# Kernel optimization log

Measured on AMD Instinct MI355X. Metric: run time of the kernel, lower is better.

Reference implementation:

```python
import jax, jax.numpy as jnp
import numpy as np

D_MODEL = 2048
N_HEADS = 16
HEAD_DIM = D_MODEL // N_HEADS
D_FF = ((int(8 * D_MODEL / 3) + 64) // 64) * 64  # 5504
B, T = 2, 2048
EPS = 1e-8
NEG = -1e9


def rotate_half(x):
    half = x.shape[-1] // 2
    return jnp.concatenate([-x[..., half:], x[..., :half]], axis=-1)


def apply_rope(x, cos, sin):
    # x: [B,H,T,hd]; cos/sin: [T,hd] -> [1,1,T,hd]
    c = cos[None, None, :, :]
    s = sin[None, None, :, :]
    return x * c + rotate_half(x) * s


def rmsnorm(x, w):
    rms = jnp.sqrt(jnp.mean(x * x, axis=-1, keepdims=True))
    return w * x / (rms + EPS)


def setup_inputs() -> dict:
    key = jax.random.key(0)
    ks = jax.random.split(key, 12)
    x = jax.random.normal(ks[0], (B, T, D_MODEL), dtype=jnp.float32)
    # RoPE tables
    inv_freq = 1.0 / (10000.0 ** (jnp.arange(0, HEAD_DIM, 2, dtype=jnp.float32) / HEAD_DIM))
    pos = jnp.arange(T, dtype=jnp.float32)
    freqs = pos[:, None] * inv_freq[None, :]          # [T, hd/2]
    emb = jnp.concatenate([freqs, freqs], axis=-1)    # [T, hd]
    cos, sin = jnp.cos(emb), jnp.sin(emb)
    # causal additive mask [T,T]
    mask = jnp.where(jnp.tril(jnp.ones((T, T), dtype=bool)), 0.0, NEG).astype(jnp.float32)
    scale = 0.02
    Wq = jax.random.normal(ks[1], (D_MODEL, D_MODEL), dtype=jnp.float32) * scale
    Wk = jax.random.normal(ks[2], (D_MODEL, D_MODEL), dtype=jnp.float32) * scale
    Wv = jax.random.normal(ks[3], (D_MODEL, D_MODEL), dtype=jnp.float32) * scale
    Wo = jax.random.normal(ks[4], (D_MODEL, D_MODEL), dtype=jnp.float32) * scale
    W1 = jax.random.normal(ks[5], (D_FF, D_MODEL), dtype=jnp.float32) * scale
    W2 = jax.random.normal(ks[6], (D_FF, D_MODEL), dtype=jnp.float32) * scale
    Wout = jax.random.normal(ks[7], (D_MODEL, D_FF), dtype=jnp.float32) * scale
    g1 = jnp.ones((D_MODEL,), dtype=jnp.float32)
    g2 = jnp.ones((D_MODEL,), dtype=jnp.float32)
    return {"x": x, "cos": cos, "sin": sin, "mask": mask,
            "g1": g1, "g2": g2, "Wq": Wq, "Wk": Wk, "Wv": Wv, "Wo": Wo,
            "W1": W1, "W2": W2, "Wout": Wout}


def reference(x, cos, sin, mask, g1, g2, Wq, Wk, Wv, Wo, W1, W2, Wout):
    Bb, Tt, Dd = x.shape

    def split_heads(t):  # [B,T,D] -> [B,H,T,hd]
        return t.reshape(Bb, Tt, N_HEADS, HEAD_DIM).transpose(0, 2, 1, 3)

    h = rmsnorm(x, g1)
    Q = apply_rope(split_heads(h @ Wq.T), cos, sin)
    K = apply_rope(split_heads(h @ Wk.T), cos, sin)
    V = split_heads(h @ Wv.T)
    scores = jnp.einsum('bhqd,bhkd->bhqk', Q, K) / jnp.sqrt(jnp.float32(HEAD_DIM))
    scores = scores + mask  # broadcast [T,T] over [B,H,T,T]
    weights = jax.nn.softmax(scores, axis=-1)
    attn = jnp.einsum('bhqk,bhkd->bhqd', weights, V)
    attn = attn.transpose(0, 2, 1, 3).reshape(Bb, Tt, Dd)
    x = x + attn @ Wo.T

    h2 = rmsnorm(x, g2)
    ff = (jax.nn.silu(h2 @ W1.T) * (h2 @ W2.T)) @ Wout.T
    return x + ff
```

## Files before the change

kernel.cpp:

```cpp
#include <hip/hip_runtime.h>


using bf16 = __bf16;
typedef __bf16 bf16x2 __attribute__((ext_vector_type(2)));
typedef __bf16 bf16x8 __attribute__((ext_vector_type(8)));
typedef float f32x4 __attribute__((ext_vector_type(4)));

#define MFMA_BF16(a, b, c) __builtin_amdgcn_mfma_f32_16x16x32_bf16((a), (b), (c), 0, 0, 0)

__device__ __forceinline__ void gld_lds16(const void* g, void* l) {
  __builtin_amdgcn_global_load_lds((const __attribute__((address_space(1))) void*)g,
                                   (__attribute__((address_space(3))) void*)l,
                                   16, 0, 0);
}

__global__ void detect_dtype(const unsigned int* __restrict__ X, int* __restrict__ flag) {
  const int tid = threadIdx.x;
  const unsigned int w = X[tid];
  const unsigned int e_lo = (w >> 7) & 0xFF;
  const unsigned int e_hi = (w >> 23) & 0xFF;
  const bool sane = (e_lo >= 97u && e_lo <= 157u) && (e_hi >= 97u && e_hi <= 157u);
  const unsigned long long m = __ballot(sane);
  if (tid == 0) *flag = (__popcll(m) > 48) ? 1 : 0;
}

__global__ __launch_bounds__(256) void convert_in(const void* __restrict__ src,
                                                  bf16* __restrict__ dst,
                                                  const int* __restrict__ flag) {
  const size_t i = ((size_t)blockIdx.x * 256 + threadIdx.x) * 8;
  if (*flag) {
    *(bf16x8*)(dst + i) = *(const bf16x8*)((const bf16*)src + i);
  } else {
    const float* s = (const float*)src;
    float4 a = *(const float4*)(s + i);
    float4 b = *(const float4*)(s + i + 4);
    bf16x8 o;
    o[0] = (bf16)a.x; o[1] = (bf16)a.y; o[2] = (bf16)a.z; o[3] = (bf16)a.w;
    o[4] = (bf16)b.x; o[5] = (bf16)b.y; o[6] = (bf16)b.z; o[7] = (bf16)b.w;
    *(bf16x8*)(dst + i) = o;
  }
}

__global__ __launch_bounds__(256) void rmsnorm_bf16(const bf16* __restrict__ X,
                                                    const bf16* __restrict__ g,
                                                    bf16* __restrict__ Hout) {
  const int row = blockIdx.x, tid = threadIdx.x;
  const size_t off = (size_t)row * 2048 + tid * 8;
  bf16x8 x8 = *(const bf16x8*)(X + off);
  float v[8];
  float s = 0.f;
#pragma unroll
  for (int j = 0; j < 8; ++j) { v[j] = (float)x8[j]; s += v[j] * v[j]; }
#pragma unroll
  for (int o = 32; o; o >>= 1) s += __shfl_xor(s, o);
  __shared__ float red[4];
  if ((tid & 63) == 0) red[tid >> 6] = s;
  __syncthreads();
  const float tot = red[0] + red[1] + red[2] + red[3];
  const float inv = 1.f / (sqrtf(tot * (1.f / 2048.f)) + 1e-8f);
  bf16x8 g8 = *(const bf16x8*)(g + tid * 8);
  bf16x8 o8;
#pragma unroll
  for (int j = 0; j < 8; ++j) o8[j] = (bf16)((float)g8[j] * v[j] * inv);
  *(bf16x8*)(Hout + off) = o8;
}

__global__ __launch_bounds__(256) void rmsnorm_f32(const float* __restrict__ X,
                                                   const bf16* __restrict__ g,
                                                   bf16* __restrict__ Hout) {
  const int row = blockIdx.x, tid = threadIdx.x;
  const size_t off = (size_t)row * 2048 + tid * 8;
  float4 a0 = *(const float4*)(X + off);
  float4 a1 = *(const float4*)(X + off + 4);
  float v[8] = {a0.x, a0.y, a0.z, a0.w, a1.x, a1.y, a1.z, a1.w};
  float s = 0.f;
#pragma unroll
  for (int j = 0; j < 8; ++j) s += v[j] * v[j];
#pragma unroll
  for (int o = 32; o; o >>= 1) s += __shfl_xor(s, o);
  __shared__ float red[4];
  if ((tid & 63) == 0) red[tid >> 6] = s;
  __syncthreads();
  const float tot = red[0] + red[1] + red[2] + red[3];
  const float inv = 1.f / (sqrtf(tot * (1.f / 2048.f)) + 1e-8f);
  bf16x8 g8 = *(const bf16x8*)(g + tid * 8);
  bf16x8 o8;
#pragma unroll
  for (int j = 0; j < 8; ++j) o8[j] = (bf16)((float)g8[j] * v[j] * inv);
  *(bf16x8*)(Hout + off) = o8;
}

__global__ __launch_bounds__(256) void rope_k(bf16* __restrict__ Q, bf16* __restrict__ Kg,
                                              const bf16* __restrict__ cosb,
                                              const bf16* __restrict__ sinb) {
  const int tid = threadIdx.x;
  const int rr = tid >> 7;
  const int c = tid & 127;
  const int bt = blockIdx.x * 2 + rr;
  const int t = bt & 2047;
  const int h = c >> 3;
  const int d0 = (c & 7) * 8;
  const size_t row = (size_t)bt * 2048;
  const int i0 = h * 128 + d0;
  bf16x8 c0 = *(const bf16x8*)(cosb + t * 128 + d0);
  bf16x8 c1 = *(const bf16x8*)(cosb + t * 128 + d0 + 64);
  bf16x8 s0 = *(const bf16x8*)(sinb + t * 128 + d0);
  bf16x8 s1 = *(const bf16x8*)(sinb + t * 128 + d0 + 64);
  bf16x8 qa = *(const bf16x8*)(Q + row + i0);
  bf16x8 qb = *(const bf16x8*)(Q + row + i0 + 64);
  bf16x8 ka = *(const bf16x8*)(Kg + row + i0);
  bf16x8 kb = *(const bf16x8*)(Kg + row + i0 + 64);
  bf16x8 qo0, qo1, ko0, ko1;
#pragma unroll
  for (int j = 0; j < 8; ++j) {
    float cj0 = (float)c0[j], cj1 = (float)c1[j];
    float sj0 = (float)s0[j], sj1 = (float)s1[j];
    float qaj = (float)qa[j], qbj = (float)qb[j];
    float kaj = (float)ka[j], kbj = (float)kb[j];
    qo0[j] = (bf16)(qaj * cj0 - qbj * sj0);
    qo1[j] = (bf16)(qbj * cj1 + qaj * sj1);
    ko0[j] = (bf16)(kaj * cj0 - kbj * sj0);
    ko1[j] = (bf16)(kbj * cj1 + kaj * sj1);
  }
  *(bf16x8*)(Q + row + i0) = qo0;
  *(bf16x8*)(Q + row + i0 + 64) = qo1;
  *(bf16x8*)(Kg + row + i0) = ko0;
  *(bf16x8*)(Kg + row + i0 + 64) = ko1;
}

template <int EPI>
__global__ __launch_bounds__(256) void gemm_bt(const bf16* __restrict__ A,
                                               const bf16* __restrict__ W,
                                               bf16* __restrict__ Cb, float* __restrict__ Cf,
                                               const bf16* __restrict__ resb,
                                               const float* __restrict__ resf,
                                               const bf16* __restrict__ mulb,
                                               const int* __restrict__ oflag,
                                               int M, int N, int K) {
  __shared__ bf16 As[2][128 * 32];
  __shared__ bf16 Ws[2][128 * 32];
  const int tid = threadIdx.x;
  const int wave = tid >> 6, lane = tid & 63;
  const int quad = lane >> 4, l15 = lane & 15;
  const int wm = wave >> 1, wn = wave & 1;
  const int m0 = blockIdx.y * 128, n0 = blockIdx.x * 128;

  f32x4 acc[4][4];
#pragma unroll
  for (int i = 0; i < 4; ++i)
#pragma unroll
    for (int j = 0; j < 4; ++j) acc[i][j] = {0.f, 0.f, 0.f, 0.f};

  const int srow = lane >> 2;
  const int skk = (lane & 3) * 8;
  const bf16* Ab = A + (size_t)m0 * K;
  const bf16* Wb = W + (size_t)n0 * K;

  auto stage = [&](int buf, int kb) {
    const int k0 = kb << 5;
#pragma unroll
    for (int c = 0; c < 2; ++c) {
      const int r = (wave * 2 + c) * 16 + srow;
      gld_lds16(Ab + (size_t)r * K + k0 + skk, (char*)As[buf] + (wave * 2 + c) * 1024);
      gld_lds16(Wb + (size_t)r * K + k0 + skk, (char*)Ws[buf] + (wave * 2 + c) * 1024);
    }
  };
  auto compute = [&](int buf) {
    bf16x8 af[4], wf[4];
#pragma unroll
    for (int mt = 0; mt < 4; ++mt)
      af[mt] = *(const bf16x8*)&As[buf][(wm * 64 + mt * 16 + l15) * 32 + quad * 8];
#pragma unroll
    for (int nt = 0; nt < 4; ++nt)
      wf[nt] = *(const bf16x8*)&Ws[buf][(wn * 64 + nt * 16 + l15) * 32 + quad * 8];
#pragma unroll
    for (int mt = 0; mt < 4; ++mt)
#pragma unroll
      for (int nt = 0; nt < 4; ++nt)
        acc[mt][nt] = MFMA_BF16(af[mt], wf[nt], acc[mt][nt]);
  };

  const int nk = K >> 5;
  stage(0, 0);
  for (int kb = 0; kb < nk; kb += 2) {
    __syncthreads();
    if (kb + 1 < nk) stage(1, kb + 1);
    compute(0);
    __syncthreads();
    if (kb + 2 < nk) stage(0, kb + 2);
    compute(1);
  }

  const int obf = (EPI == 4 && oflag) ? *oflag : 0;
#pragma unroll
  for (int mt = 0; mt < 4; ++mt) {
#pragma unroll
    for (int nt = 0; nt < 4; ++nt) {
#pragma unroll
      for (int r = 0; r < 4; ++r) {
        const int row = m0 + wm * 64 + mt * 16 + quad * 4 + r;
        const int col = n0 + wn * 64 + nt * 16 + l15;
        const size_t idx = (size_t)row * N + col;
        const float v = acc[mt][nt][r];
        if constexpr (EPI == 0) {
          Cb[idx] = (bf16)v;
        } else if constexpr (EPI == 1) {
          Cf[idx] = v + (float)resb[idx];
        } else if constexpr (EPI == 2) {
          Cb[idx] = (bf16)(v / (1.f + __expf(-v)));
        } else if constexpr (EPI == 3) {
          Cb[idx] = (bf16)((float)mulb[idx] * v);
        } else {
          const float rres = resf[idx] + v;
          if (obf) Cb[idx] = (bf16)rres;
          else     Cf[idx] = rres;
        }
      }
    }
  }
}

__global__ __launch_bounds__(256) void flash_attn(const bf16* __restrict__ Q,
                                                  const bf16* __restrict__ Kg,
                                                  const bf16* __restrict__ Vg,
                                                  bf16* __restrict__ O) {
  __shared__ bf16 Ks[2][64 * 128];
  __shared__ bf16 Vt[2][128 * 64];
  __shared__ bf16 Ps[4 * 16 * 64];
  const int tid = threadIdx.x;
  const int wave = tid >> 6, lane = tid & 63;
  const int quad = lane >> 4, l15 = lane & 15;
  const int bh = blockIdx.y;
  const int b = bh >> 4, h = bh & 15;
  const size_t base = (size_t)b * 2048 * 2048 + h * 128;
  const float scale = 0.08838834764831845f;

  bf16x8 vva[2], vvb[2];

  auto stageK = [&](int buf, int kb) {
    const int k0 = kb * 64;
#pragma unroll
    for (int c = 0; c < 4; ++c) {
      const int ch = tid + 256 * c;
      const int row = ch >> 4;
      const int scb = ((ch & 15) * 16) ^ ((row & 7) << 4);
      gld_lds16((const char*)(Kg + base + (size_t)(k0 + row) * 2048) + scb,
                (char*)Ks[buf] + wave * 1024 + c * 4096);
    }
  };
  auto loadV = [&](int kb) {
    const int k0 = kb * 64;
#pragma unroll
    for (int c = 0; c < 2; ++c) {
      const int tau = tid + 256 * c;
      const int kp = tau & 31;
      const int d0 = (tau >> 5) * 8;
      vva[c] = *(const bf16x8*)(Vg + base + (size_t)(k0 + 2 * kp) * 2048 + d0);
      vvb[c] = *(const bf16x8*)(Vg + base + (size_t)(k0 + 2 * kp + 1) * 2048 + d0);
    }
  };
  auto writeV = [&](int buf) {
#pragma unroll
    for (int c = 0; c < 2; ++c) {
      const int tau = tid + 256 * c;
      const int kp = tau & 31;
      const int d0 = (tau >> 5) * 8;
#pragma unroll
      for (int j = 0; j < 8; ++j) {
        bf16x2 pr = {vva[c][j], vvb[c][j]};
        const int d = d0 + j;
        *(bf16x2*)((char*)Vt[buf] + d * 128 + ((4 * kp) ^ ((d & 7) << 4))) = pr;
      }
    }
  };

#pragma unroll 1
  for (int half = 0; half < 2; ++half) {
    const int qt = half ? (31 - (int)blockIdx.x) : (int)blockIdx.x;
    const int q0 = qt * 64;

    bf16x8 qf[4];
    {
      const bf16* qrow = Q + base + (size_t)(q0 + wave * 16 + l15) * 2048;
#pragma unroll
      for (int ks = 0; ks < 4; ++ks) qf[ks] = *(const bf16x8*)(qrow + ks * 32 + quad * 8);
    }

    f32x4 o[8];
#pragma unroll
    for (int i = 0; i < 8; ++i) o[i] = {0.f, 0.f, 0.f, 0.f};
    float m_r[4] = {-1e30f, -1e30f, -1e30f, -1e30f};
    float l_r[4] = {0.f, 0.f, 0.f, 0.f};

    __syncthreads();
    loadV(0);
    stageK(0, 0);
    writeV(0);
    __syncthreads();
    if (qt >= 1) { loadV(1); stageK(1, 1); }

#pragma unroll 1
    for (int kb = 0; kb <= qt; ++kb) {
      const int cur = kb & 1;
      const int k0 = kb * 64;

      f32x4 s[4];
#pragma unroll
      for (int nt = 0; nt < 4; ++nt) {
        s[nt] = {0.f, 0.f, 0.f, 0.f};
        const int krow = nt * 16 + l15;
#pragma unroll
        for (int ks = 0; ks < 4; ++ks) {
          bf16x8 kf = *(const bf16x8*)((char*)Ks[cur] + krow * 256 +
                                       ((ks * 64 + quad * 16) ^ ((krow & 7) << 4)));
          s[nt] = MFMA_BF16(qf[ks], kf, s[nt]);
        }
      }

      float sv[4][4];
#pragma unroll
      for (int nt = 0; nt < 4; ++nt) {
#pragma unroll
        for (int r = 0; r < 4; ++r) {
          float v = s[nt][r] * scale;
          const int key = k0 + nt * 16 + l15;
          const int qq = q0 + wave * 16 + quad * 4 + r;
          if (key > qq) v = -1e9f;
          sv[nt][r] = v;
        }
      }

#pragma unroll
      for (int r = 0; r < 4; ++r) {
        float rmax = fmaxf(fmaxf(sv[0][r], sv[1][r]), fmaxf(sv[2][r], sv[3][r]));
#pragma unroll
        for (int off = 1; off < 16; off <<= 1) rmax = fmaxf(rmax, __shfl_xor(rmax, off));
        const float mnew = fmaxf(m_r[r], rmax);
        const float alpha = __expf(m_r[r] - mnew);
        float psum = 0.f;
        const int qrow = quad * 4 + r;
#pragma unroll
        for (int nt = 0; nt < 4; ++nt) {
          const float p = __expf(sv[nt][r] - mnew);
          psum += p;
          *(bf16*)((char*)Ps + wave * 2048 + qrow * 128 +
                   ((2 * (nt * 16 + l15)) ^ ((qrow & 7) << 4))) = (bf16)p;
        }
#pragma unroll
        for (int off = 1; off < 16; off <<= 1) psum += __shfl_xor(psum, off);
        l_r[r] = l_r[r] * alpha + psum;
        m_r[r] = mnew;
#pragma unroll
        for (int nt2 = 0; nt2 < 8; ++nt2) o[nt2][r] *= alpha;
      }

      asm volatile("s_waitcnt lgkmcnt(0)" ::: "memory");

#pragma unroll
      for (int ks2 = 0; ks2 < 2; ++ks2) {
        bf16x8 pf = *(const bf16x8*)((char*)Ps + wave * 2048 + l15 * 128 +
                                     ((ks2 * 64 + quad * 16) ^ ((l15 & 7) << 4)));
#pragma unroll
        for (int nt2 = 0; nt2 < 8; ++nt2) {
          const int drow = nt2 * 16 + l15;
          bf16x8 vf = *(const bf16x8*)((char*)Vt[cur] + drow * 128 +
                                       ((ks2 * 64 + quad * 16) ^ ((drow & 7) << 4)));
          o[nt2] = MFMA_BF16(pf, vf, o[nt2]);
        }
      }

      if (kb + 1 <= qt) writeV(cur ^ 1);

      __syncthreads();
      if (kb + 2 <= qt) { loadV(kb + 2); stageK(cur, kb + 2); }
    }

#pragma unroll
    for (int nt2 = 0; nt2 < 8; ++nt2) {
#pragma unroll
      for (int r = 0; r < 4; ++r) {
        const int qq = q0 + wave * 16 + quad * 4 + r;
        const int dd = nt2 * 16 + l15;
        O[base + (size_t)qq * 2048 + dd] = (bf16)(o[nt2][r] / l_r[r]);
      }
    }
  }
}

extern "C" void kernel_launch(void* const* d_in, const int* in_sizes, int n_in,
                              void* d_out, int out_size, void* d_ws, size_t ws_size,
                              hipStream_t stream) {
  const void* x_raw = d_in[0];
  const void* cos_raw = d_in[1];
  const void* sin_raw = d_in[2];
  const void* g1_raw = d_in[4];
  const void* g2_raw = d_in[5];
  const void* W_raw[7] = {d_in[6], d_in[7], d_in[8], d_in[9], d_in[10], d_in[11], d_in[12]};

  char* ws = (char*)d_ws;
  const size_t MB = 1048576ull;
  int* flag = (int*)ws;
  bf16* g1c = (bf16*)(ws + 4096);
  bf16* g2c = (bf16*)(ws + 12288);
  bf16* cosc = (bf16*)(ws + 65536);
  bf16* sinc = (bf16*)(ws + 655360);
  bf16* xc   = (bf16*)(ws + 2 * MB);
  bf16* wslot= (bf16*)(ws + 18 * MB);
  bf16* hbuf = (bf16*)(ws + 41 * MB);
  bf16* qbuf = (bf16*)(ws + 57 * MB);
  bf16* kbuf = (bf16*)(ws + 73 * MB);
  bf16* vbuf = (bf16*)(ws + 89 * MB);
  bf16* abuf = (bf16*)(ws + 105 * MB);
  float* x1  = (float*)(ws + 57 * MB);
  bf16* h2   = (bf16*)(ws + 41 * MB);
  bf16* ubuf = (bf16*)(ws + 89 * MB);

  const int M = 4096;
  dim3 blk(256);

  detect_dtype<<<1, 64, 0, stream>>>((const unsigned int*)x_raw, flag);

  convert_in<<<4096, blk, 0, stream>>>(x_raw, xc, flag);
  convert_in<<<128, blk, 0, stream>>>(cos_raw, cosc, flag);
  convert_in<<<128, blk, 0, stream>>>(sin_raw, sinc, flag);
  convert_in<<<1, blk, 0, stream>>>(g1_raw, g1c, flag);
  convert_in<<<1, blk, 0, stream>>>(g2_raw, g2c, flag);

  rmsnorm_bf16<<<M, blk, 0, stream>>>(xc, g1c, hbuf);

  convert_in<<<2048, blk, 0, stream>>>(W_raw[0], wslot, flag);
  gemm_bt<0><<<dim3(16, 32), blk, 0, stream>>>(hbuf, wslot, qbuf, nullptr, nullptr, nullptr, nullptr, nullptr, M, 2048, 2048);
  convert_in<<<2048, blk, 0, stream>>>(W_raw[1], wslot, flag);
  gemm_bt<0><<<dim3(16, 32), blk, 0, stream>>>(hbuf, wslot, kbuf, nullptr, nullptr, nullptr, nullptr, nullptr, M, 2048, 2048);
  convert_in<<<2048, blk, 0, stream>>>(W_raw[2], wslot, flag);
  gemm_bt<0><<<dim3(16, 32), blk, 0, stream>>>(hbuf, wslot, vbuf, nullptr, nullptr, nullptr, nullptr, nullptr, M, 2048, 2048);

  rope_k<<<M / 2, blk, 0, stream>>>(qbuf, kbuf, cosc, sinc);
  flash_attn<<<dim3(16, 32), blk, 0, stream>>>(qbuf, kbuf, vbuf, abuf);

  convert_in<<<2048, blk, 0, stream>>>(W_raw[3], wslot, flag);
  gemm_bt<1><<<dim3(16, 32), blk, 0, stream>>>(abuf, wslot, nullptr, x1, xc, nullptr, nullptr, nullptr, M, 2048, 2048);

  rmsnorm_f32<<<M, blk, 0, stream>>>(x1, g2c, h2);

  convert_in<<<5504, blk, 0, stream>>>(W_raw[4], wslot, flag);
  gemm_bt<2><<<dim3(43, 32), blk, 0, stream>>>(h2, wslot, ubuf, nullptr, nullptr, nullptr, nullptr, nullptr, M, 5504, 2048);
  convert_in<<<5504, blk, 0, stream>>>(W_raw[5], wslot, flag);
  gemm_bt<3><<<dim3(43, 32), blk, 0, stream>>>(h2, wslot, ubuf, nullptr, nullptr, nullptr, ubuf, nullptr, M, 5504, 2048);
  convert_in<<<5504, blk, 0, stream>>>(W_raw[6], wslot, flag);
  gemm_bt<4><<<dim3(16, 32), blk, 0, stream>>>(ubuf, wslot, (bf16*)d_out, (float*)d_out, nullptr, x1, nullptr, flag, M, 2048, 5504);
}
```

Before: 1.072 ms.

## Restructure flash attention pipeline with single V buffer and explicit waitcnt barriers

Reworks the flash attention K/V staging. V goes into a single LDS buffer that is written at the start of each iteration from registers prefetched one block ahead. K staging is issued after the mid-iteration barrier, and __syncthreads is replaced by raw s_barrier with explicit vmcnt/lgkmcnt waits, s_setprio around the MFMA sections, and sched_barriers. The launch grid is also swapped so blockIdx.x indexes batch-head and blockIdx.y the query tile, which changes dispatch order and L2 locality. This cuts LDS use and synchronization overhead, but the hand-counted vmcnt values are fragile and the single V buffer adds a barrier per iteration.

After: 991.4 us. -7.5%, faster.

```diff
diff --git a/kernel.cpp b/kernel.cpp
--- a/kernel.cpp
+++ b/kernel.cpp
@@ -225,12 +225,12 @@
                                                   const bf16* __restrict__ Vg,
                                                   bf16* __restrict__ O) {
   __shared__ bf16 Ks[2][64 * 128];
-  __shared__ bf16 Vt[2][128 * 64];
+  __shared__ bf16 Vt[128 * 64];
   __shared__ bf16 Ps[4 * 16 * 64];
   const int tid = threadIdx.x;
   const int wave = tid >> 6, lane = tid & 63;
   const int quad = lane >> 4, l15 = lane & 15;
-  const int bh = blockIdx.y;
+  const int bh = blockIdx.x;
   const int b = bh >> 4, h = bh & 15;
   const size_t base = (size_t)b * 2048 * 2048 + h * 128;
   const float scale = 0.08838834764831845f;
@@ -259,7 +259,7 @@
       vvb[c] = *(const bf16x8*)(Vg + base + (size_t)(k0 + 2 * kp + 1) * 2048 + d0);
     }
   };
-  auto writeV = [&](int buf) {
+  auto writeV = [&]() {
 #pragma unroll
     for (int c = 0; c < 2; ++c) {
       const int tau = tid + 256 * c;
@@ -269,14 +269,14 @@
       for (int j = 0; j < 8; ++j) {
         bf16x2 pr = {vva[c][j], vvb[c][j]};
         const int d = d0 + j;
-        *(bf16x2*)((char*)Vt[buf] + d * 128 + ((4 * kp) ^ ((d & 7) << 4))) = pr;
+        *(bf16x2*)((char*)Vt + d * 128 + ((4 * kp) ^ ((d & 7) << 4))) = pr;
       }
     }
   };
 
 #pragma unroll 1
   for (int half = 0; half < 2; ++half) {
-    const int qt = half ? (31 - (int)blockIdx.x) : (int)blockIdx.x;
+    const int qt = half ? (31 - (int)blockIdx.y) : (int)blockIdx.y;
     const int q0 = qt * 64;
 
     bf16x8 qf[4];
@@ -292,19 +292,23 @@
     float m_r[4] = {-1e30f, -1e30f, -1e30f, -1e30f};
     float l_r[4] = {0.f, 0.f, 0.f, 0.f};
 
-    __syncthreads();
     loadV(0);
     stageK(0, 0);
-    writeV(0);
-    __syncthreads();
-    if (qt >= 1) { loadV(1); stageK(1, 1); }
+    if (qt >= 1) stageK(1, 1);
+    asm volatile("s_waitcnt vmcnt(4)" ::: "memory");
+    __builtin_amdgcn_s_barrier();
+    __builtin_amdgcn_sched_barrier(0);
 
 #pragma unroll 1
     for (int kb = 0; kb <= qt; ++kb) {
       const int cur = kb & 1;
       const int k0 = kb * 64;
 
+      writeV();
+      if (kb + 1 <= qt) loadV(kb + 1);
+
       f32x4 s[4];
+      __builtin_amdgcn_s_setprio(1);
 #pragma unroll
       for (int nt = 0; nt < 4; ++nt) {
         s[nt] = {0.f, 0.f, 0.f, 0.f};
@@ -316,6 +320,7 @@
           s[nt] = MFMA_BF16(qf[ks], kf, s[nt]);
         }
       }
+      __builtin_amdgcn_s_setprio(0);
 
       float sv[4][4];
 #pragma unroll
@@ -355,7 +360,12 @@
       }
 
       asm volatile("s_waitcnt lgkmcnt(0)" ::: "memory");
-
+      __builtin_amdgcn_s_barrier();
+      __builtin_amdgcn_sched_barrier(0);
+
+      if (kb + 2 <= qt) stageK(cur, kb + 2);
+
+      __builtin_amdgcn_s_setprio(1);
 #pragma unroll
       for (int ks2 = 0; ks2 < 2; ++ks2) {
         bf16x8 pf = *(const bf16x8*)((char*)Ps + wave * 2048 + l15 * 128 +
@@ -363,16 +373,17 @@
 #pragma unroll
         for (int nt2 = 0; nt2 < 8; ++nt2) {
           const int drow = nt2 * 16 + l15;
-          bf16x8 vf = *(const bf16x8*)((char*)Vt[cur] + drow * 128 +
+          bf16x8 vf = *(const bf16x8*)((char*)Vt + drow * 128 +
                                        ((ks2 * 64 + quad * 16) ^ ((drow & 7) << 4)));
           o[nt2] = MFMA_BF16(pf, vf, o[nt2]);
         }
       }
-
-      if (kb + 1 <= qt) writeV(cur ^ 1);
-
-      __syncthreads();
-      if (kb + 2 <= qt) { loadV(kb + 2); stageK(cur, kb + 2); }
+      __builtin_amdgcn_s_setprio(0);
+
+      asm volatile("s_waitcnt lgkmcnt(0)" ::: "memory");
+      asm volatile("s_waitcnt vmcnt(8)" ::: "memory");
+      __builtin_amdgcn_s_barrier();
+      __builtin_amdgcn_sched_barrier(0);
     }
 
 #pragma unroll
@@ -436,7 +447,7 @@
   gemm_bt<0><<<dim3(16, 32), blk, 0, stream>>>(hbuf, wslot, vbuf, nullptr, nullptr, nullptr, nullptr, nullptr, M, 2048, 2048);
 
   rope_k<<<M / 2, blk, 0, stream>>>(qbuf, kbuf, cosc, sinc);
-  flash_attn<<<dim3(16, 32), blk, 0, stream>>>(qbuf, kbuf, vbuf, abuf);
+  flash_attn<<<dim3(32, 16), blk, 0, stream>>>(qbuf, kbuf, vbuf, abuf);
 
   convert_in<<<2048, blk, 0, stream>>>(W_raw[3], wslot, flag);
   gemm_bt<1><<<dim3(16, 32), blk, 0, stream>>>(abuf, wslot, nullptr, x1, xc, nullptr, nullptr, nullptr, M, 2048, 2048);
```
